# Kernel tuning notes

Hardware: AMD Instinct MI355X
Metric: run time of the kernel (lower is better)

The kernel has to match this reference:

```python
import jax, jax.numpy as jnp
import numpy as np

PADDED = 1024  # 1 << (768-1).bit_length()


def fast_wht(x, N):
    """Fast Walsh-Hadamard Transform over last dim. x: [B, N], N power of 2."""
    h = x
    step = 1
    while step < N:  # log2(N) fixed iterations (unrolled under jit)
        num_groups = N // (2 * step)
        h = h.reshape(-1, num_groups, 2, step)
        a = h[:, :, 0, :]
        b = h[:, :, 1, :]
        h = jnp.stack([a + b, a - b], axis=2).reshape(-1, N)
        step *= 2
    return h / N


def setup_inputs() -> dict:
    key = jax.random.key(0)
    k1, k2, k3 = jax.random.split(key, 3)
    B, N, D = 8, 4096, 768
    x = jax.random.normal(k1, (B, N, D), dtype=jnp.float32)
    wht_weight = jax.random.normal(k2, (PADDED,), dtype=jnp.float32)
    gate_w = jax.random.normal(k3, (D, PADDED), dtype=jnp.float32) * 0.02
    gate_b = jnp.ones((D,), dtype=jnp.float32)
    return {"x": x, "wht_weight": wht_weight, "gate_w": gate_w, "gate_b": gate_b}


def reference(x, wht_weight, gate_w, gate_b):
    B, N, D = x.shape
    c = x.mean(axis=1)                                  # [B, D] global average pool
    pad = PADDED - D
    c_pad = jnp.pad(c, ((0, 0), (0, pad))) if pad > 0 else c  # [B, PADDED]
    c_wht = fast_wht(c_pad, PADDED)                     # [B, PADDED]
    c_weighted = c_wht * wht_weight                     # [B, PADDED]
    gate = jax.nn.sigmoid(c_weighted @ gate_w.T + gate_b)  # [B, D]
    return x * gate[:, None, :]                         # [B, N, D]
```

## Files before the change

kernel.cpp:

```cpp
#include <hip/hip_runtime.h>
#include <math.h>

#define Bb 8
#define Nn 4096
#define Dd 768
#define PADDED 1024
#define D4 192
#define NCHUNK 64
#define ROWS (Nn / NCHUNK)

__global__ void k_colsum_part(const float4* __restrict__ x4, float* __restrict__ partial) {
    int bid = blockIdx.x;
    int b = bid >> 6;
    int k = bid & (NCHUNK - 1);
    int t = threadIdx.x;
    const float4* p = x4 + ((size_t)(b * Nn + k * ROWS) * D4) + t;
    float4 acc = {0.f, 0.f, 0.f, 0.f};
#pragma unroll 8
    for (int r = 0; r < ROWS; ++r) {
        float4 v = p[(size_t)r * D4];
        acc.x += v.x; acc.y += v.y; acc.z += v.z; acc.w += v.w;
    }
    float4* dst = (float4*)(partial + ((size_t)k * Bb + b) * Dd) + t;
    *dst = acc;
}

__global__ void k_colsum_atomic(const float4* __restrict__ x4, float* __restrict__ c_sum) {
    int bid = blockIdx.x;
    int b = bid >> 6;
    int k = bid & (NCHUNK - 1);
    int t = threadIdx.x;
    const float4* p = x4 + ((size_t)(b * Nn + k * ROWS) * D4) + t;
    float4 acc = {0.f, 0.f, 0.f, 0.f};
#pragma unroll 8
    for (int r = 0; r < ROWS; ++r) {
        float4 v = p[(size_t)r * D4];
        acc.x += v.x; acc.y += v.y; acc.z += v.z; acc.w += v.w;
    }
    float* cs = c_sum + b * Dd + t * 4;
    atomicAdd(cs + 0, acc.x);
    atomicAdd(cs + 1, acc.y);
    atomicAdd(cs + 2, acc.z);
    atomicAdd(cs + 3, acc.w);
}

__global__ void k_wht(const float* __restrict__ src, int nchunks,
                      const float* __restrict__ wht_weight,
                      float* __restrict__ cw) {
    __shared__ float s[PADDED];
    int b = blockIdx.x;
    int t = threadIdx.x;
    float v = 0.f;
    if (t < Dd) {
        float acc = 0.f;
        for (int k = 0; k < nchunks; ++k)
            acc += src[((size_t)k * Bb + b) * Dd + t];
        v = acc * (1.0f / (float)Nn);
    }
    s[t] = v;
    __syncthreads();
    for (int st = 1; st < PADDED; st <<= 1) {
        float a = s[t];
        float p = s[t ^ st];
        __syncthreads();
        s[t] = (t & st) ? (p - a) : (a + p);
        __syncthreads();
    }
    cw[b * PADDED + t] = s[t] * (1.0f / (float)PADDED) * wht_weight[t];
}

__global__ void k_gate(const float* __restrict__ cw, const float4* __restrict__ gw4,
                       const float* __restrict__ gate_b, float* __restrict__ gate) {
    __shared__ float s[PADDED];
    int b = blockIdx.y;
    int dchunk = blockIdx.x;
    int t = threadIdx.x;
    for (int i = t; i < PADDED; i += 256) s[i] = cw[b * PADDED + i];
    __syncthreads();
    int d = dchunk * 256 + t;
    const float4* w = gw4 + (size_t)d * (PADDED / 4);
    float acc = 0.f;
#pragma unroll 8
    for (int p = 0; p < PADDED / 4; ++p) {
        float4 wv = w[p];
        acc += s[4 * p] * wv.x + s[4 * p + 1] * wv.y
             + s[4 * p + 2] * wv.z + s[4 * p + 3] * wv.w;
    }
    float tsum = acc + gate_b[d];
    gate[b * Dd + d] = 1.0f / (1.0f + expf(-tsum));
}

__global__ void k_scale(const float4* __restrict__ x4, const float4* __restrict__ gate4,
                        float4* __restrict__ out4) {
    int bid = blockIdx.x;
    int b = bid >> 8;
    int n0 = (bid & 255) * 16;
    int t = threadIdx.x;
    float4 g = gate4[b * D4 + t];
    size_t base = ((size_t)(b * Nn + n0) * D4) + t;
#pragma unroll
    for (int r = 0; r < 16; ++r) {
        float4 v = x4[base + (size_t)r * D4];
        float4 o;
        o.x = v.x * g.x; o.y = v.y * g.y; o.z = v.z * g.z; o.w = v.w * g.w;
        out4[base + (size_t)r * D4] = o;
    }
}

extern "C" void kernel_launch(void* const* d_in, const int* in_sizes, int n_in,
                              void* d_out, int out_size, void* d_ws, size_t ws_size,
                              hipStream_t stream) {
    const float* x          = (const float*)d_in[0];
    const float* wht_weight = (const float*)d_in[1];
    const float* gate_w     = (const float*)d_in[2];
    const float* gate_b     = (const float*)d_in[3];
    float* out = (float*)d_out;

    size_t need_big = ((size_t)NCHUNK * Bb * Dd + (size_t)Bb * PADDED + (size_t)Bb * Dd) * 4;
    float* wsf = (float*)d_ws;

    if (ws_size >= need_big) {
        float* partial = wsf;
        float* cw   = partial + (size_t)NCHUNK * Bb * Dd;
        float* gate = cw + (size_t)Bb * PADDED;
        k_colsum_part<<<Bb * NCHUNK, 192, 0, stream>>>((const float4*)x, partial);
        k_wht<<<Bb, PADDED, 0, stream>>>(partial, NCHUNK, wht_weight, cw);
        k_gate<<<dim3(3, Bb), 256, 0, stream>>>(cw, (const float4*)gate_w, gate_b, gate);
        k_scale<<<Bb * 256, 192, 0, stream>>>((const float4*)x, (const float4*)gate, (float4*)out);
    } else {
        float* c_sum = wsf;
        float* cw    = c_sum + (size_t)Bb * Dd;
        float* gate  = cw + (size_t)Bb * PADDED;
        hipMemsetAsync(c_sum, 0, (size_t)Bb * Dd * sizeof(float), stream);
        k_colsum_atomic<<<Bb * NCHUNK, 192, 0, stream>>>((const float4*)x, c_sum);
        k_wht<<<Bb, PADDED, 0, stream>>>(c_sum, 1, wht_weight, cw);
        k_gate<<<dim3(3, Bb), 256, 0, stream>>>(cw, (const float4*)gate_w, gate_b, gate);
        k_scale<<<Bb * 256, 192, 0, stream>>>((const float4*)x, (const float4*)gate, (float4*)out);
    }
}
```

Baseline: 245.6 us.

## Fuse WHT and gate matvec, double colsum chunks, nontemporal output stores

Merges the WHT kernel and gate matvec kernel into one 1024-thread block per batch, removing a launch and the cw round-trip. Doubles the number of column-sum chunks to raise parallelism in the reduction pass. The scale kernel now uses native vector types and nontemporal stores for the output. The fused gate matvec runs on only 8 blocks instead of 24, which may lengthen that stage.

```diff
diff --git a/kernel.cpp b/kernel.cpp
--- a/kernel.cpp
+++ b/kernel.cpp
@@ -6,12 +6,15 @@
 #define Dd 768
 #define PADDED 1024
 #define D4 192
-#define NCHUNK 64
+#define NCHUNK 128
 #define ROWS (Nn / NCHUNK)
 
-__global__ void k_colsum_part(const float4* __restrict__ x4, float* __restrict__ partial) {
+typedef float floatx4 __attribute__((ext_vector_type(4)));
+
+__global__ __launch_bounds__(192) void k_colsum_part(const float4* __restrict__ x4,
+                                                     float* __restrict__ partial) {
     int bid = blockIdx.x;
-    int b = bid >> 6;
+    int b = bid >> 7;
     int k = bid & (NCHUNK - 1);
     int t = threadIdx.x;
     const float4* p = x4 + ((size_t)(b * Nn + k * ROWS) * D4) + t;
@@ -25,9 +28,10 @@
     *dst = acc;
 }
 
-__global__ void k_colsum_atomic(const float4* __restrict__ x4, float* __restrict__ c_sum) {
+__global__ __launch_bounds__(192) void k_colsum_atomic(const float4* __restrict__ x4,
+                                                       float* __restrict__ c_sum) {
     int bid = blockIdx.x;
-    int b = bid >> 6;
+    int b = bid >> 7;
     int k = bid & (NCHUNK - 1);
     int t = threadIdx.x;
     const float4* p = x4 + ((size_t)(b * Nn + k * ROWS) * D4) + t;
@@ -44,9 +48,11 @@
     atomicAdd(cs + 3, acc.w);
 }
 
-__global__ void k_wht(const float* __restrict__ src, int nchunks,
-                      const float* __restrict__ wht_weight,
-                      float* __restrict__ cw) {
+__global__ __launch_bounds__(PADDED) void k_whtgate(const float* __restrict__ src, int nchunks,
+                                                    const float* __restrict__ wht_weight,
+                                                    const float4* __restrict__ gw4,
+                                                    const float* __restrict__ gate_b,
+                                                    float* __restrict__ gate) {
     __shared__ float s[PADDED];
     int b = blockIdx.x;
     int t = threadIdx.x;
@@ -66,44 +72,36 @@
         s[t] = (t & st) ? (p - a) : (a + p);
         __syncthreads();
     }
-    cw[b * PADDED + t] = s[t] * (1.0f / (float)PADDED) * wht_weight[t];
+    s[t] = s[t] * (1.0f / (float)PADDED) * wht_weight[t];
+    __syncthreads();
+    if (t < Dd) {
+        const float4* w = gw4 + (size_t)t * (PADDED / 4);
+        float acc = 0.f;
+#pragma unroll 8
+        for (int p = 0; p < PADDED / 4; ++p) {
+            float4 wv = w[p];
+            acc += s[4 * p] * wv.x + s[4 * p + 1] * wv.y
+                 + s[4 * p + 2] * wv.z + s[4 * p + 3] * wv.w;
+        }
+        float z = acc + gate_b[t];
+        gate[b * Dd + t] = 1.0f / (1.0f + expf(-z));
+    }
 }
 
-__global__ void k_gate(const float* __restrict__ cw, const float4* __restrict__ gw4,
-                       const float* __restrict__ gate_b, float* __restrict__ gate) {
-    __shared__ float s[PADDED];
-    int b = blockIdx.y;
-    int dchunk = blockIdx.x;
-    int t = threadIdx.x;
-    for (int i = t; i < PADDED; i += 256) s[i] = cw[b * PADDED + i];
-    __syncthreads();
-    int d = dchunk * 256 + t;
-    const float4* w = gw4 + (size_t)d * (PADDED / 4);
-    float acc = 0.f;
-#pragma unroll 8
-    for (int p = 0; p < PADDED / 4; ++p) {
-        float4 wv = w[p];
-        acc += s[4 * p] * wv.x + s[4 * p + 1] * wv.y
-             + s[4 * p + 2] * wv.z + s[4 * p + 3] * wv.w;
-    }
-    float tsum = acc + gate_b[d];
-    gate[b * Dd + d] = 1.0f / (1.0f + expf(-tsum));
-}
-
-__global__ void k_scale(const float4* __restrict__ x4, const float4* __restrict__ gate4,
-                        float4* __restrict__ out4) {
+__global__ __launch_bounds__(192) void k_scale(const floatx4* __restrict__ x4,
+                                               const floatx4* __restrict__ gate4,
+                                               floatx4* __restrict__ out4) {
     int bid = blockIdx.x;
     int b = bid >> 8;
     int n0 = (bid & 255) * 16;
     int t = threadIdx.x;
-    float4 g = gate4[b * D4 + t];
+    floatx4 g = gate4[b * D4 + t];
     size_t base = ((size_t)(b * Nn + n0) * D4) + t;
 #pragma unroll
     for (int r = 0; r < 16; ++r) {
-        float4 v = x4[base + (size_t)r * D4];
-        float4 o;
-        o.x = v.x * g.x; o.y = v.y * g.y; o.z = v.z * g.z; o.w = v.w * g.w;
-        out4[base + (size_t)r * D4] = o;
+        floatx4 v = x4[base + (size_t)r * D4];
+        floatx4 o = v * g;
+        __builtin_nontemporal_store(o, &out4[base + (size_t)r * D4]);
     }
 }
 
@@ -116,25 +114,23 @@
     const float* gate_b     = (const float*)d_in[3];
     float* out = (float*)d_out;
 
-    size_t need_big = ((size_t)NCHUNK * Bb * Dd + (size_t)Bb * PADDED + (size_t)Bb * Dd) * 4;
+    size_t need_big = ((size_t)NCHUNK * Bb * Dd + (size_t)Bb * Dd) * 4;
     float* wsf = (float*)d_ws;
 
     if (ws_size >= need_big) {
         float* partial = wsf;
-        float* cw   = partial + (size_t)NCHUNK * Bb * Dd;
-        float* gate = cw + (size_t)Bb * PADDED;
+        float* gate = partial + (size_t)NCHUNK * Bb * Dd;
         k_colsum_part<<<Bb * NCHUNK, 192, 0, stream>>>((const float4*)x, partial);
-        k_wht<<<Bb, PADDED, 0, stream>>>(partial, NCHUNK, wht_weight, cw);
-        k_gate<<<dim3(3, Bb), 256, 0, stream>>>(cw, (const float4*)gate_w, gate_b, gate);
-        k_scale<<<Bb * 256, 192, 0, stream>>>((const float4*)x, (const float4*)gate, (float4*)out);
+        k_whtgate<<<Bb, PADDED, 0, stream>>>(partial, NCHUNK, wht_weight,
+                                             (const float4*)gate_w, gate_b, gate);
+        k_scale<<<Bb * 256, 192, 0, stream>>>((const floatx4*)x, (const floatx4*)gate, (floatx4*)out);
     } else {
         float* c_sum = wsf;
-        float* cw    = c_sum + (size_t)Bb * Dd;
-        float* gate  = cw + (size_t)Bb * PADDED;
-        hipMemsetAsync(c_sum, 0, (size_t)Bb * Dd * sizeof(float), stream);
+        float* gate  = c_sum + (size_t)Bb * Dd;
+        (void)hipMemsetAsync(c_sum, 0, (size_t)Bb * Dd * sizeof(float), stream);
         k_colsum_atomic<<<Bb * NCHUNK, 192, 0, stream>>>((const float4*)x, c_sum);
-        k_wht<<<Bb, PADDED, 0, stream>>>(c_sum, 1, wht_weight, cw);
-        k_gate<<<dim3(3, Bb), 256, 0, stream>>>(cw, (const float4*)gate_w, gate_b, gate);
-        k_scale<<<Bb * 256, 192, 0, stream>>>((const float4*)x, (const float4*)gate, (float4*)out);
+        k_whtgate<<<Bb, PADDED, 0, stream>>>(c_sum, 1, wht_weight,
+                                             (const float4*)gate_w, gate_b, gate);
+        k_scale<<<Bb * 256, 192, 0, stream>>>((const floatx4*)x, (const floatx4*)gate, (floatx4*)out);
     }
 }
```

Measured after the change: 314.9 us. 1.28x slower.
